# Kernel tuning notes

Measured on AMD Instinct MI355X. Metric: run time of the kernel, lower is better.

Reference implementation:

```python
import jax, jax.numpy as jnp
import numpy as np

B, D, K = 32768, 256, 2048
BETA = 0.25


def setup_inputs() -> dict:
    key = jax.random.key(0)
    k1, k2 = jax.random.split(key)
    latents = jax.random.normal(k1, (B, D), dtype=jnp.float32)
    # nn.Embedding weight initialized uniform(-1/K, 1/K)
    embedding = jax.random.uniform(k2, (K, D), dtype=jnp.float32,
                                   minval=-1.0 / K, maxval=1.0 / K)
    return {"latents": latents, "embedding": embedding}


def reference(latents, embedding):
    # Squared-L2 distances: [B, K]
    dist = (jnp.sum(latents ** 2, axis=1, keepdims=True)
            + jnp.sum(embedding ** 2, axis=1)
            - 2.0 * jnp.matmul(latents, embedding.T))
    encoding_inds = jnp.argmin(dist, axis=1)  # [B]

    # Gather codebook rows (equivalent to one-hot @ embedding)
    quantized = embedding[encoding_inds]  # [B, D]

    commitment_loss = jnp.mean((jax.lax.stop_gradient(quantized) - latents) ** 2)
    embedding_loss = jnp.mean((quantized - jax.lax.stop_gradient(latents)) ** 2)
    vq_loss = commitment_loss * BETA + embedding_loss

    # Straight-through estimator
    quantized_st = latents + jax.lax.stop_gradient(quantized - latents)

    # avg_probs = mean of one-hot over batch == normalized histogram of inds
    counts = jnp.zeros((K,), dtype=jnp.float32).at[encoding_inds].add(1.0)
    avg_probs = counts / B
    entropy_vq = -jnp.sum(avg_probs * jnp.log(avg_probs + 1e-10))

    # dist values at selected codes
    cluster_metric = jnp.mean(
        jnp.take_along_axis(dist, encoding_inds[:, None], axis=1))

    return (quantized_st, vq_loss, entropy_vq,
            encoding_inds[:, None], cluster_metric)
```

## Files before the change

### kernel.cpp

```cpp
#include <hip/hip_runtime.h>
#include <math.h>

#define B_ROWS 32768
#define D_DIM  256
#define K_CODES 2048

#define OUT_Q   0
#define OUT_VQ  8388608
#define OUT_ENT 8388609
#define OUT_IND 8388610
#define OUT_CM  8421378


#define WS_SE2   0
#define WS_SX2   8192
#define WS_CNT   139264
#define WS_PACK  147456
#define WS_MSEP  409600
#define WS_DISTP 475136
#define WS_BCAT  540672

typedef _Float16 f16x8 __attribute__((ext_vector_type(8)));
typedef float f32x4 __attribute__((ext_vector_type(4)));
typedef union { _Float16 h[4]; uint2 u2; } h4pack;

__global__ __launch_bounds__(256) void k_init(
    const float* __restrict__ X, const float* __restrict__ E,
    _Float16* __restrict__ A, _Float16* __restrict__ Bc,
    float* __restrict__ sx2, float* __restrict__ se2,
    unsigned long long* __restrict__ packed, int* __restrict__ counts) {
  int w = threadIdx.x >> 6, lane = threadIdx.x & 63;
  if (blockIdx.x < 8192) {
    int row = blockIdx.x * 4 + w;
    float4 v = ((const float4*)(X + (size_t)row * D_DIM))[lane];
    float s = v.x * v.x + v.y * v.y + v.z * v.z + v.w * v.w;
#pragma unroll
    for (int off = 32; off > 0; off >>= 1) s += __shfl_xor(s, off, 64);
    if (lane == 0) { sx2[row] = s; packed[row] = ~0ull; }
    h4pack hi, lo;
    hi.h[0] = (_Float16)v.x; hi.h[1] = (_Float16)v.y;
    hi.h[2] = (_Float16)v.z; hi.h[3] = (_Float16)v.w;
    lo.h[0] = (_Float16)((v.x - (float)hi.h[0]) * 4096.0f);
    lo.h[1] = (_Float16)((v.y - (float)hi.h[1]) * 4096.0f);
    lo.h[2] = (_Float16)((v.z - (float)hi.h[2]) * 4096.0f);
    lo.h[3] = (_Float16)((v.w - (float)hi.h[3]) * 4096.0f);
    *(uint2*)&A[(size_t)row * 512 + 4 * lane] = hi.u2;
    *(uint2*)&A[(size_t)row * 512 + 256 + 4 * lane] = lo.u2;
  } else {
    int bb = blockIdx.x - 8192;
    int row = bb * 4 + w;
    if (threadIdx.x < 4) counts[bb * 4 + threadIdx.x] = 0;
    float4 v = ((const float4*)(E + (size_t)row * D_DIM))[lane];
    float s = v.x * v.x + v.y * v.y + v.z * v.z + v.w * v.w;
#pragma unroll
    for (int off = 32; off > 0; off >>= 1) s += __shfl_xor(s, off, 64);
    if (lane == 0) se2[row] = s;
    const float S = 4194304.0f;
    const float SH = 0.000244140625f;
    float e0 = v.x * S, e1 = v.y * S, e2 = v.z * S, e3 = v.w * S;
    h4pack b1, b2, b3;
    b1.h[0] = (_Float16)e0; b1.h[1] = (_Float16)e1;
    b1.h[2] = (_Float16)e2; b1.h[3] = (_Float16)e3;
    b2.h[0] = (_Float16)((float)b1.h[0] * SH);
    b2.h[1] = (_Float16)((float)b1.h[1] * SH);
    b2.h[2] = (_Float16)((float)b1.h[2] * SH);
    b2.h[3] = (_Float16)((float)b1.h[3] * SH);
    b3.h[0] = (_Float16)(e0 - (float)b1.h[0]);
    b3.h[1] = (_Float16)(e1 - (float)b1.h[1]);
    b3.h[2] = (_Float16)(e2 - (float)b1.h[2]);
    b3.h[3] = (_Float16)(e3 - (float)b1.h[3]);
    *(uint2*)&Bc[(size_t)row * 768 + 4 * lane] = b1.u2;
    *(uint2*)&Bc[(size_t)row * 768 + 256 + 4 * lane] = b2.u2;
    *(uint2*)&Bc[(size_t)row * 768 + 512 + 4 * lane] = b3.u2;
  }
}

#define BAR()  __builtin_amdgcn_s_barrier()
#define SB0()  __builtin_amdgcn_sched_barrier(0)
#define WLGKM0()                                                \
  do {                                                          \
    asm volatile("s_waitcnt lgkmcnt(0)" ::: "memory");          \
    SB0();                                                      \
  } while (0)
#define DSR(dst, a, o) \
  asm volatile("ds_read_b128 %0, %1 offset:" o : "=v"(dst) : "v"(a))

#define MFMA_QUAD(I0, J0, BF)                                                \
  do {                                                                       \
    __builtin_amdgcn_s_setprio(1);                                           \
    _Pragma("unroll") for (int ii = 0; ii < 4; ++ii) {                       \
      _Pragma("unroll") for (int jj = 0; jj < 2; ++jj) {                     \
        _Pragma("unroll") for (int kk = 0; kk < 2; ++kk) {                   \
          acc[(I0) + ii][(J0) + jj] =                                        \
              __builtin_amdgcn_mfma_f32_16x16x32_f16(                        \
                  af[ii * 2 + kk], (BF)[jj * 2 + kk],                        \
                  acc[(I0) + ii][(J0) + jj], 0, 0, 0);                       \
        }                                                                    \
      }                                                                      \
    }                                                                        \
    __builtin_amdgcn_s_setprio(0);                                           \
  } while (0)

__global__ __launch_bounds__(512, 2) void k_mfma2(
    const _Float16* __restrict__ A, const _Float16* __restrict__ Bc,
    const float* __restrict__ se2, const float* __restrict__ sx2,
    unsigned long long* __restrict__ packed) {
  extern __shared__ char smem[];
  const int tid = threadIdx.x;
  const int w = tid >> 6, lane = tid & 63;
  const int wm = w >> 2, wn = w & 3;
  const int q = lane >> 4, c = lane & 15;
  const int rowb = blockIdx.x & 127, colb = blockIdx.x >> 7;
  const int rowpan = rowb * 256, colpan = colb * 256;
  const int rsel = lane >> 3;
  const int chunkb = ((lane & 7) ^ rsel) * 16;
  const int rswz = c & 7;

  const char* Abase = (const char*)A;
  const char* Bbase = (const char*)Bc;

  auto issue = [&](int tt, int g, int bsel) {
    const int hh = (g == 3 || g == 4 || g == 5 || g == 7) ? 1 : 0;
    const int ss = (g == 2 || g == 4 || g == 6 || g == 7) ? 1 : 0;
    const int rl = hh * 128 + ss * 64 + w * 8 + rsel;
    const char* src;
    char* dst;
    if (g == 0 || g >= 5) {
      int aoff = (tt & 3) * 128 + (((tt >> 2) == 1) ? 512 : 0);
      src = Abase + ((size_t)(rowpan + rl) << 10) + aoff + chunkb;
      dst = smem + bsel * 32768 + hh * 16384 + ss * 8192 + w * 1024;
    } else {
      src = Bbase + (size_t)(colpan + rl) * 1536 + tt * 128 + chunkb;
      dst = smem + 65536 + bsel * 32768 + hh * 16384 + ss * 8192 + w * 1024;
    }
    __builtin_amdgcn_global_load_lds(
        (const __attribute__((address_space(1))) unsigned int*)src,
        (__attribute__((address_space(3))) unsigned int*)dst, 16, 0, 0);
  };

  f32x4 acc[8][4];
#pragma unroll
  for (int i = 0; i < 8; ++i)
#pragma unroll
    for (int j = 0; j < 4; ++j) acc[i][j] = (f32x4){0.f, 0.f, 0.f, 0.f};

  const unsigned ldsA = (unsigned)(uintptr_t)smem + (unsigned)((wm * 128 + c) * 128);
  const unsigned ldsB = (unsigned)(uintptr_t)smem + 65536u +
                        (unsigned)((wn * 64 + c) * 128);
  const unsigned sl0 = (unsigned)(((0 * 4 + q) ^ rswz) * 16);
  const unsigned sl1 = (unsigned)(((1 * 4 + q) ^ rswz) * 16);

#pragma unroll
  for (int g = 0; g < 8; ++g) issue(0, g, 0);
  asm volatile("s_waitcnt vmcnt(2)" ::: "memory");
  BAR();

  f16x8 af[8], bf01[4], bf23[4];

  for (int t = 0; t < 12; ++t) {
    const int bsel = t & 1;
    const int nb = bsel ^ 1;
    const bool pre = (t < 11);
    const unsigned aA0 = ldsA + (unsigned)(bsel * 32768) + sl0;
    const unsigned aA1 = ldsA + (unsigned)(bsel * 32768) + sl1;
    const unsigned aB0 = ldsB + (unsigned)(bsel * 32768) + sl0;
    const unsigned aB1 = ldsB + (unsigned)(bsel * 32768) + sl1;

    if (pre) { issue(t + 1, 0, nb); issue(t + 1, 1, nb); }
    DSR(af[0], aA0, "0");    DSR(af[1], aA1, "0");
    DSR(af[2], aA0, "2048"); DSR(af[3], aA1, "2048");
    DSR(af[4], aA0, "4096"); DSR(af[5], aA1, "4096");
    DSR(af[6], aA0, "6144"); DSR(af[7], aA1, "6144");
    DSR(bf01[0], aB0, "0");    DSR(bf01[1], aB1, "0");
    DSR(bf01[2], aB0, "2048"); DSR(bf01[3], aB1, "2048");
    BAR();
    WLGKM0();
    MFMA_QUAD(0, 0, bf01);
    SB0();
    BAR();

    if (pre) { issue(t + 1, 2, nb); issue(t + 1, 3, nb); }
    DSR(bf23[0], aB0, "4096"); DSR(bf23[1], aB1, "4096");
    DSR(bf23[2], aB0, "6144"); DSR(bf23[3], aB1, "6144");
    BAR();
    WLGKM0();
    MFMA_QUAD(0, 2, bf23);
    SB0();
    if (pre) asm volatile("s_waitcnt vmcnt(4)" ::: "memory");
    else     asm volatile("s_waitcnt vmcnt(0)" ::: "memory");
    BAR();

    if (pre) { issue(t + 1, 4, nb); issue(t + 1, 5, nb); }
    DSR(af[0], aA0, "8192");  DSR(af[1], aA1, "8192");
    DSR(af[2], aA0, "10240"); DSR(af[3], aA1, "10240");
    DSR(af[4], aA0, "12288"); DSR(af[5], aA1, "12288");
    DSR(af[6], aA0, "14336"); DSR(af[7], aA1, "14336");
    BAR();
    WLGKM0();
    MFMA_QUAD(4, 2, bf23);
    SB0();
    if (pre) { issue(t + 1, 6, nb); issue(t + 1, 7, nb); }
    MFMA_QUAD(4, 0, bf01);
    SB0();
    if (pre) asm volatile("s_waitcnt vmcnt(2)" ::: "memory");
    BAR();
  }

  __syncthreads();

  const float inv = 4.76837158203125e-07f;
  float se_j[4];
#pragma unroll
  for (int j = 0; j < 4; ++j) se_j[j] = se2[colpan + wn * 64 + j * 16 + c];
  unsigned long long* m = (unsigned long long*)smem;
#pragma unroll
  for (int i = 0; i < 8; ++i) {
    float4 sx4 = *(const float4*)&sx2[rowpan + wm * 128 + i * 16 + q * 4];
#pragma unroll
    for (int r = 0; r < 4; ++r) {
      float sx = ((const float*)&sx4)[r];
      float bs = 3.402823466e38f;
      int bk = 0;
#pragma unroll
      for (int j = 0; j < 4; ++j) {
        float t1 = sx + se_j[j];
        float d = t1 - acc[i][j][r] * inv;
        if (d < bs) { bs = d; bk = colpan + wn * 64 + j * 16 + c; }
      }
#pragma unroll
      for (int off = 1; off < 16; off <<= 1) {
        float os = __shfl_xor(bs, off, 64);
        int ok = __shfl_xor(bk, off, 64);
        if (os < bs || (os == bs && ok < bk)) { bs = os; bk = ok; }
      }
      if (c == 0) {
        m[wn * 256 + wm * 128 + i * 16 + q * 4 + r] =
            ((unsigned long long)__float_as_uint(bs) << 32) |
            (unsigned long long)(unsigned int)bk;
      }
    }
  }
  __syncthreads();
  if (tid < 256) {
    unsigned long long v = m[tid];
#pragma unroll
    for (int mm = 1; mm < 4; ++mm) {
      unsigned long long o = m[mm * 256 + tid];
      if (o < v) v = o;
    }
    atomicMin(&packed[rowpan + tid], v);
  }
}

__global__ __launch_bounds__(256) void k_gather(
    const float* __restrict__ X, const float* __restrict__ E,
    const unsigned long long* __restrict__ packed, float* __restrict__ outq,
    float* __restrict__ out_ind, int* __restrict__ counts,
    double* __restrict__ msep, double* __restrict__ distp) {
  __shared__ int sk[16];
  __shared__ float sd[16];
  int tid = threadIdx.x;
  if (tid < 16) {
    int row = blockIdx.x * 16 + tid;
    unsigned long long v = packed[row];
    int k = (int)(v & 0xFFFFFFFFull);
    sk[tid] = k;
    sd[tid] = __uint_as_float((unsigned int)(v >> 32));
    out_ind[row] = (float)k;
    atomicAdd(&counts[k], 1);
  }
  __syncthreads();
  int wave = tid >> 6, lane = tid & 63;
  double msum = 0.0, dsum = 0.0;
#pragma unroll
  for (int rr = 0; rr < 4; rr++) {
    int li = wave * 4 + rr;
    int b = blockIdx.x * 16 + li;
    int ind = sk[li];
    float4 x4 = ((const float4*)(X + (size_t)b * D_DIM))[lane];
    float4 q4 = ((const float4*)(E + (size_t)ind * D_DIM))[lane];
    float d0 = q4.x - x4.x, d1 = q4.y - x4.y, d2 = q4.z - x4.z, d3 = q4.w - x4.w;
    float4 o;
    o.x = x4.x + d0; o.y = x4.y + d1; o.z = x4.z + d2; o.w = x4.w + d3;
    ((float4*)(outq + (size_t)b * D_DIM))[lane] = o;
    float v = d0 * d0 + d1 * d1 + d2 * d2 + d3 * d3;
#pragma unroll
    for (int off = 32; off > 0; off >>= 1) v += __shfl_xor(v, off, 64);
    if (lane == 0) { msum += (double)v; dsum += (double)sd[li]; }
  }
  if (lane == 0) {
    int wg = blockIdx.x * 4 + wave;
    msep[wg] = msum;
    distp[wg] = dsum;
  }
}

__global__ __launch_bounds__(256) void k_final(
    const int* __restrict__ counts, const double* __restrict__ msep,
    const double* __restrict__ distp, float* __restrict__ out) {
  __shared__ double red[256];
  int t = threadIdx.x;

  double m = 0.0;
  for (int i = t; i < 8192; i += 256) m += msep[i];
  red[t] = m;
  __syncthreads();
  for (int s = 128; s > 0; s >>= 1) {
    if (t < s) red[t] += red[t + s];
    __syncthreads();
  }
  if (t == 0) {
    double mse = red[0] / ((double)B_ROWS * (double)D_DIM);
    out[OUT_VQ] = (float)(mse * 1.25);
  }
  __syncthreads();

  double d = 0.0;
  for (int i = t; i < 8192; i += 256) d += distp[i];
  red[t] = d;
  __syncthreads();
  for (int s = 128; s > 0; s >>= 1) {
    if (t < s) red[t] += red[t + s];
    __syncthreads();
  }
  if (t == 0) out[OUT_CM] = (float)(red[0] / (double)B_ROWS);
  __syncthreads();

  double e = 0.0;
  for (int k = t; k < K_CODES; k += 256) {
    float p = (float)counts[k] * (1.0f / 32768.0f);
    e += (double)(p * logf(p + 1e-10f));
  }
  red[t] = e;
  __syncthreads();
  for (int s = 128; s > 0; s >>= 1) {
    if (t < s) red[t] += red[t + s];
    __syncthreads();
  }
  if (t == 0) out[OUT_ENT] = (float)(-red[0]);
}

extern "C" void kernel_launch(void* const* d_in, const int* in_sizes, int n_in,
                              void* d_out, int out_size, void* d_ws,
                              size_t ws_size, hipStream_t stream) {
  const float* X = (const float*)d_in[0];
  const float* E = (const float*)d_in[1];
  float* out = (float*)d_out;
  char* ws = (char*)d_ws;
  float* se2 = (float*)(ws + WS_SE2);
  float* sx2 = (float*)(ws + WS_SX2);
  int* counts = (int*)(ws + WS_CNT);
  unsigned long long* packed = (unsigned long long*)(ws + WS_PACK);
  double* msep = (double*)(ws + WS_MSEP);
  double* distp = (double*)(ws + WS_DISTP);
  _Float16* Bcat = (_Float16*)(ws + WS_BCAT);
  _Float16* Acat = (_Float16*)d_out;

  static bool attr_done = false;
  if (!attr_done) {
    hipFuncSetAttribute((const void*)k_mfma2,
                        hipFuncAttributeMaxDynamicSharedMemorySize, 131072);
    attr_done = true;
  }

  k_init<<<8704, 256, 0, stream>>>(X, E, Acat, Bcat, sx2, se2, packed, counts);
  k_mfma2<<<1024, 512, 131072, stream>>>(Acat, Bcat, se2, sx2, packed);
  k_gather<<<B_ROWS / 16, 256, 0, stream>>>(X, E, packed, out + OUT_Q,
                                            out + OUT_IND, counts, msep, distp);
  k_final<<<1, 256, 0, stream>>>(counts, msep, distp, out);
}
```

Before: 258.7 us.

## Restructure MFMA main loop to one barrier per k-step with bulk prefetch

```diff
diff --git a/kernel.cpp b/kernel.cpp
--- a/kernel.cpp
+++ b/kernel.cpp
@@ -77,15 +77,15 @@
 
 #define BAR()  __builtin_amdgcn_s_barrier()
 #define SB0()  __builtin_amdgcn_sched_barrier(0)
-#define WLGKM0()                                                \
-  do {                                                          \
-    asm volatile("s_waitcnt lgkmcnt(0)" ::: "memory");          \
-    SB0();                                                      \
+#define WLGKM(n)                                                 \
+  do {                                                           \
+    asm volatile("s_waitcnt lgkmcnt(" #n ")" ::: "memory");      \
+    SB0();                                                       \
   } while (0)
 #define DSR(dst, a, o) \
   asm volatile("ds_read_b128 %0, %1 offset:" o : "=v"(dst) : "v"(a))
 
-#define MFMA_QUAD(I0, J0, BF)                                                \
+#define MFMA_QUAD(I0, J0, AF, BF)                                            \
   do {                                                                       \
     __builtin_amdgcn_s_setprio(1);                                           \
     _Pragma("unroll") for (int ii = 0; ii < 4; ++ii) {                       \
@@ -93,7 +93,7 @@
         _Pragma("unroll") for (int kk = 0; kk < 2; ++kk) {                   \
           acc[(I0) + ii][(J0) + jj] =                                        \
               __builtin_amdgcn_mfma_f32_16x16x32_f16(                        \
-                  af[ii * 2 + kk], (BF)[jj * 2 + kk],                        \
+                  (AF)[ii * 2 + kk], (BF)[jj * 2 + kk],                      \
                   acc[(I0) + ii][(J0) + jj], 0, 0, 0);                       \
         }                                                                    \
       }                                                                      \
@@ -152,58 +152,51 @@
 
 #pragma unroll
   for (int g = 0; g < 8; ++g) issue(0, g, 0);
-  asm volatile("s_waitcnt vmcnt(2)" ::: "memory");
+  asm volatile("s_waitcnt vmcnt(0)" ::: "memory");
   BAR();
 
   f16x8 af[8], bf01[4], bf23[4];
 
+#pragma unroll 2
   for (int t = 0; t < 12; ++t) {
     const int bsel = t & 1;
-    const int nb = bsel ^ 1;
     const bool pre = (t < 11);
     const unsigned aA0 = ldsA + (unsigned)(bsel * 32768) + sl0;
     const unsigned aA1 = ldsA + (unsigned)(bsel * 32768) + sl1;
     const unsigned aB0 = ldsB + (unsigned)(bsel * 32768) + sl0;
     const unsigned aB1 = ldsB + (unsigned)(bsel * 32768) + sl1;
 
-    if (pre) { issue(t + 1, 0, nb); issue(t + 1, 1, nb); }
+    if (pre) {
+#pragma unroll
+      for (int g = 0; g < 8; ++g) issue(t + 1, g, bsel ^ 1);
+    }
+
     DSR(af[0], aA0, "0");    DSR(af[1], aA1, "0");
     DSR(af[2], aA0, "2048"); DSR(af[3], aA1, "2048");
     DSR(af[4], aA0, "4096"); DSR(af[5], aA1, "4096");
     DSR(af[6], aA0, "6144"); DSR(af[7], aA1, "6144");
     DSR(bf01[0], aB0, "0");    DSR(bf01[1], aB1, "0");
     DSR(bf01[2], aB0, "2048"); DSR(bf01[3], aB1, "2048");
-    BAR();
-    WLGKM0();
-    MFMA_QUAD(0, 0, bf01);
-    SB0();
-    BAR();
-
-    if (pre) { issue(t + 1, 2, nb); issue(t + 1, 3, nb); }
     DSR(bf23[0], aB0, "4096"); DSR(bf23[1], aB1, "4096");
     DSR(bf23[2], aB0, "6144"); DSR(bf23[3], aB1, "6144");
-    BAR();
-    WLGKM0();
-    MFMA_QUAD(0, 2, bf23);
-    SB0();
-    if (pre) asm volatile("s_waitcnt vmcnt(4)" ::: "memory");
-    else     asm volatile("s_waitcnt vmcnt(0)" ::: "memory");
-    BAR();
-
-    if (pre) { issue(t + 1, 4, nb); issue(t + 1, 5, nb); }
+
+    WLGKM(4);
+    MFMA_QUAD(0, 0, af, bf01);
+    WLGKM(0);
+    MFMA_QUAD(0, 2, af, bf23);
+
     DSR(af[0], aA0, "8192");  DSR(af[1], aA1, "8192");
     DSR(af[2], aA0, "10240"); DSR(af[3], aA1, "10240");
     DSR(af[4], aA0, "12288"); DSR(af[5], aA1, "12288");
     DSR(af[6], aA0, "14336"); DSR(af[7], aA1, "14336");
-    BAR();
-    WLGKM0();
-    MFMA_QUAD(4, 2, bf23);
-    SB0();
-    if (pre) { issue(t + 1, 6, nb); issue(t + 1, 7, nb); }
-    MFMA_QUAD(4, 0, bf01);
-    SB0();
-    if (pre) asm volatile("s_waitcnt vmcnt(2)" ::: "memory");
-    BAR();
+    WLGKM(0);
+    MFMA_QUAD(4, 2, af, bf23);
+    MFMA_QUAD(4, 0, af, bf01);
+
+    if (pre) {
+      asm volatile("s_waitcnt vmcnt(0)" ::: "memory");
+      BAR();
+    }
   }
 
   __syncthreads();
```

Measured after the change: 261.9 us. No clear change (+1.3%).

## Fuse final reduction into gather via last-block counter and reorder MFMA prefetch issue

Applied to the files above, without the earlier changes.

```diff
diff --git a/kernel.cpp b/kernel.cpp
--- a/kernel.cpp
+++ b/kernel.cpp
@@ -82,10 +82,11 @@
     asm volatile("s_waitcnt lgkmcnt(0)" ::: "memory");          \
     SB0();                                                      \
   } while (0)
+#define VMW(n) asm volatile("s_waitcnt vmcnt(" #n ")" ::: "memory")
 #define DSR(dst, a, o) \
   asm volatile("ds_read_b128 %0, %1 offset:" o : "=v"(dst) : "v"(a))
 
-#define MFMA_QUAD(I0, J0, BF)                                                \
+#define MFMA_QUAD(I0, J0, AF, BF)                                            \
   do {                                                                       \
     __builtin_amdgcn_s_setprio(1);                                           \
     _Pragma("unroll") for (int ii = 0; ii < 4; ++ii) {                       \
@@ -93,20 +94,22 @@
         _Pragma("unroll") for (int kk = 0; kk < 2; ++kk) {                   \
           acc[(I0) + ii][(J0) + jj] =                                        \
               __builtin_amdgcn_mfma_f32_16x16x32_f16(                        \
-                  af[ii * 2 + kk], (BF)[jj * 2 + kk],                        \
+                  (AF)[ii * 2 + kk], (BF)[jj * 2 + kk],                      \
                   acc[(I0) + ii][(J0) + jj], 0, 0, 0);                       \
         }                                                                    \
       }                                                                      \
     }                                                                        \
     __builtin_amdgcn_s_setprio(0);                                           \
+    SB0();                                                                   \
   } while (0)
 
 __global__ __launch_bounds__(512, 2) void k_mfma2(
     const _Float16* __restrict__ A, const _Float16* __restrict__ Bc,
     const float* __restrict__ se2, const float* __restrict__ sx2,
-    unsigned long long* __restrict__ packed) {
+    unsigned long long* __restrict__ packed, float* __restrict__ outbase) {
   extern __shared__ char smem[];
   const int tid = threadIdx.x;
+  if (blockIdx.x == 0 && tid == 0) *(unsigned*)(outbase + OUT_VQ) = 0u;
   const int w = tid >> 6, lane = tid & 63;
   const int wm = w >> 2, wn = w & 3;
   const int q = lane >> 4, c = lane & 15;
@@ -152,11 +155,12 @@
 
 #pragma unroll
   for (int g = 0; g < 8; ++g) issue(0, g, 0);
-  asm volatile("s_waitcnt vmcnt(2)" ::: "memory");
+  VMW(2);
   BAR();
 
   f16x8 af[8], bf01[4], bf23[4];
 
+#pragma unroll 2
   for (int t = 0; t < 12; ++t) {
     const int bsel = t & 1;
     const int nb = bsel ^ 1;
@@ -166,43 +170,40 @@
     const unsigned aB0 = ldsB + (unsigned)(bsel * 32768) + sl0;
     const unsigned aB1 = ldsB + (unsigned)(bsel * 32768) + sl1;
 
-    if (pre) { issue(t + 1, 0, nb); issue(t + 1, 1, nb); }
     DSR(af[0], aA0, "0");    DSR(af[1], aA1, "0");
     DSR(af[2], aA0, "2048"); DSR(af[3], aA1, "2048");
     DSR(af[4], aA0, "4096"); DSR(af[5], aA1, "4096");
     DSR(af[6], aA0, "6144"); DSR(af[7], aA1, "6144");
     DSR(bf01[0], aB0, "0");    DSR(bf01[1], aB1, "0");
     DSR(bf01[2], aB0, "2048"); DSR(bf01[3], aB1, "2048");
+    if (pre) { issue(t + 1, 0, nb); issue(t + 1, 1, nb); }
     BAR();
     WLGKM0();
-    MFMA_QUAD(0, 0, bf01);
-    SB0();
-    BAR();
-
-    if (pre) { issue(t + 1, 2, nb); issue(t + 1, 3, nb); }
+    MFMA_QUAD(0, 0, af, bf01);
+    BAR();
+
     DSR(bf23[0], aB0, "4096"); DSR(bf23[1], aB1, "4096");
     DSR(bf23[2], aB0, "6144"); DSR(bf23[3], aB1, "6144");
+    if (pre) { issue(t + 1, 2, nb); issue(t + 1, 3, nb); }
     BAR();
     WLGKM0();
-    MFMA_QUAD(0, 2, bf23);
-    SB0();
-    if (pre) asm volatile("s_waitcnt vmcnt(4)" ::: "memory");
-    else     asm volatile("s_waitcnt vmcnt(0)" ::: "memory");
-    BAR();
-
-    if (pre) { issue(t + 1, 4, nb); issue(t + 1, 5, nb); }
+    MFMA_QUAD(0, 2, af, bf23);
+    if (pre) VMW(4); else VMW(0);
+    BAR();
+
     DSR(af[0], aA0, "8192");  DSR(af[1], aA1, "8192");
     DSR(af[2], aA0, "10240"); DSR(af[3], aA1, "10240");
     DSR(af[4], aA0, "12288"); DSR(af[5], aA1, "12288");
     DSR(af[6], aA0, "14336"); DSR(af[7], aA1, "14336");
+    if (pre) { issue(t + 1, 4, nb); issue(t + 1, 5, nb); }
     BAR();
     WLGKM0();
-    MFMA_QUAD(4, 2, bf23);
-    SB0();
+    MFMA_QUAD(4, 2, af, bf23);
+    BAR();
+
     if (pre) { issue(t + 1, 6, nb); issue(t + 1, 7, nb); }
-    MFMA_QUAD(4, 0, bf01);
-    SB0();
-    if (pre) asm volatile("s_waitcnt vmcnt(2)" ::: "memory");
+    MFMA_QUAD(4, 0, af, bf01);
+    if (pre) VMW(2);
     BAR();
   }
 
@@ -254,11 +255,12 @@
 
 __global__ __launch_bounds__(256) void k_gather(
     const float* __restrict__ X, const float* __restrict__ E,
-    const unsigned long long* __restrict__ packed, float* __restrict__ outq,
-    float* __restrict__ out_ind, int* __restrict__ counts,
-    double* __restrict__ msep, double* __restrict__ distp) {
+    const unsigned long long* __restrict__ packed, float* __restrict__ out,
+    int* __restrict__ counts, double* __restrict__ msep,
+    double* __restrict__ distp) {
   __shared__ int sk[16];
   __shared__ float sd[16];
+  __shared__ int lastflag;
   int tid = threadIdx.x;
   if (tid < 16) {
     int row = blockIdx.x * 16 + tid;
@@ -266,7 +268,7 @@
     int k = (int)(v & 0xFFFFFFFFull);
     sk[tid] = k;
     sd[tid] = __uint_as_float((unsigned int)(v >> 32));
-    out_ind[row] = (float)k;
+    out[OUT_IND + row] = (float)k;
     atomicAdd(&counts[k], 1);
   }
   __syncthreads();
@@ -282,7 +284,7 @@
     float d0 = q4.x - x4.x, d1 = q4.y - x4.y, d2 = q4.z - x4.z, d3 = q4.w - x4.w;
     float4 o;
     o.x = x4.x + d0; o.y = x4.y + d1; o.z = x4.z + d2; o.w = x4.w + d3;
-    ((float4*)(outq + (size_t)b * D_DIM))[lane] = o;
+    ((float4*)(out + OUT_Q + (size_t)b * D_DIM))[lane] = o;
     float v = d0 * d0 + d1 * d1 + d2 * d2 + d3 * d3;
 #pragma unroll
     for (int off = 32; off > 0; off >>= 1) v += __shfl_xor(v, off, 64);
@@ -293,51 +295,53 @@
     msep[wg] = msum;
     distp[wg] = dsum;
   }
-}
-
-__global__ __launch_bounds__(256) void k_final(
-    const int* __restrict__ counts, const double* __restrict__ msep,
-    const double* __restrict__ distp, float* __restrict__ out) {
+
+  __threadfence();
+  __syncthreads();
+  if (tid == 0)
+    lastflag = (atomicAdd((unsigned*)(out + OUT_VQ), 1u) == 2047u);
+  __syncthreads();
+  if (!lastflag) return;
+  __threadfence();
+
   __shared__ double red[256];
-  int t = threadIdx.x;
-
   double m = 0.0;
-  for (int i = t; i < 8192; i += 256) m += msep[i];
-  red[t] = m;
+  for (int i = tid; i < 8192; i += 256) m += msep[i];
+  red[tid] = m;
   __syncthreads();
   for (int s = 128; s > 0; s >>= 1) {
-    if (t < s) red[t] += red[t + s];
+    if (tid < s) red[tid] += red[tid + s];
     __syncthreads();
   }
-  if (t == 0) {
+  if (tid == 0) {
     double mse = red[0] / ((double)B_ROWS * (double)D_DIM);
     out[OUT_VQ] = (float)(mse * 1.25);
   }
   __syncthreads();
 
   double d = 0.0;
-  for (int i = t; i < 8192; i += 256) d += distp[i];
-  red[t] = d;
+  for (int i = tid; i < 8192; i += 256) d += distp[i];
+  red[tid] = d;
   __syncthreads();
   for (int s = 128; s > 0; s >>= 1) {
-    if (t < s) red[t] += red[t + s];
+    if (tid < s) red[tid] += red[tid + s];
     __syncthreads();
   }
-  if (t == 0) out[OUT_CM] = (float)(red[0] / (double)B_ROWS);
+  if (tid == 0) out[OUT_CM] = (float)(red[0] / (double)B_ROWS);
   __syncthreads();
 
   double e = 0.0;
-  for (int k = t; k < K_CODES; k += 256) {
+  for (int k = tid; k < K_CODES; k += 256) {
     float p = (float)counts[k] * (1.0f / 32768.0f);
     e += (double)(p * logf(p + 1e-10f));
   }
-  red[t] = e;
+  red[tid] = e;
   __syncthreads();
   for (int s = 128; s > 0; s >>= 1) {
-    if (t < s) red[t] += red[t + s];
+    if (tid < s) red[tid] += red[tid + s];
     __syncthreads();
   }
-  if (t == 0) out[OUT_ENT] = (float)(-red[0]);
+  if (tid == 0) out[OUT_ENT] = (float)(-red[0]);
 }
 
 extern "C" void kernel_launch(void* const* d_in, const int* in_sizes, int n_in,
@@ -364,8 +368,7 @@
   }
 
   k_init<<<8704, 256, 0, stream>>>(X, E, Acat, Bcat, sx2, se2, packed, counts);
-  k_mfma2<<<1024, 512, 131072, stream>>>(Acat, Bcat, se2, sx2, packed);
-  k_gather<<<B_ROWS / 16, 256, 0, stream>>>(X, E, packed, out + OUT_Q,
-                                            out + OUT_IND, counts, msep, distp);
-  k_final<<<1, 256, 0, stream>>>(counts, msep, distp, out);
+  k_mfma2<<<1024, 512, 131072, stream>>>(Acat, Bcat, se2, sx2, packed, out);
+  k_gather<<<B_ROWS / 16, 256, 0, stream>>>(X, E, packed, out, counts, msep,
+                                            distp);
 }
```

After: 477.6 us. 84.6% more time.
